# Kernel optimization log

Hardware: AMD Instinct MI355X
Metric: run time of the kernel (lower is better)

## Reference

```python
import jax, jax.numpy as jnp
import numpy as np

WS = 3          # window size (odd)
NH = 8          # num heads
EPS = 1e-5      # LayerNorm eps (torch default)


def _ln(x, g, b):
    mu = x.mean(-1, keepdims=True)
    var = ((x - mu) ** 2).mean(-1, keepdims=True)
    return (x - mu) / jnp.sqrt(var + EPS) * g + b


def _neighbors(x, ws):
    # x: [B,D,H,W,C] -> [B,D,H,W,ws^3,C] zero-padded cubic neighborhoods
    B, D, H, W, C = x.shape
    r = ws // 2
    xp = jnp.pad(x, ((0, 0), (r, r), (r, r), (r, r), (0, 0)))
    slabs = [xp[:, i:i + D, j:j + H, k:k + W, :]
             for i in range(ws) for j in range(ws) for k in range(ws)]
    return jnp.stack(slabs, axis=4)


def _mask(D, H, W, ws):
    # True for valid (in-bounds, non-center) neighbors: [D,H,W,ws^3]
    r = ws // 2
    valid = jnp.pad(jnp.ones((D, H, W), dtype=bool), ((r, r), (r, r), (r, r)))
    slabs = [valid[i:i + D, j:j + H, k:k + W]
             for i in range(ws) for j in range(ws) for k in range(ws)]
    m = jnp.stack(slabs, axis=3)
    center = r * ws * ws + r * ws + r  # self voxel is masked out
    return m.at[..., center].set(False)


def setup_inputs() -> dict:
    key = jax.random.key(0)
    ks = jax.random.split(key, 18)
    B, D, H, W, C = 2, 16, 16, 16, 256
    F = 4 * C
    s = 0.02
    inp = {
        "x": jax.random.normal(ks[0], (B, D, H, W, C), jnp.float32),
        "Wq": jax.random.normal(ks[1], (C, C), jnp.float32) * s,
        "bq": jnp.zeros((C,), jnp.float32),
        "Wk": jax.random.normal(ks[2], (C, C), jnp.float32) * s,
        "bk": jnp.zeros((C,), jnp.float32),
        "Wv": jax.random.normal(ks[3], (C, C), jnp.float32) * s,
        "bv": jnp.zeros((C,), jnp.float32),
        "Wo": jax.random.normal(ks[4], (C, C), jnp.float32) * s,
        "bo": jnp.zeros((C,), jnp.float32),
        "g1": jnp.ones((C,), jnp.float32),
        "b1": jnp.zeros((C,), jnp.float32),
        "g2": jnp.ones((C,), jnp.float32),
        "b2": jnp.zeros((C,), jnp.float32),
        "W1": jax.random.normal(ks[5], (C, F), jnp.float32) * s,
        "bf1": jnp.zeros((F,), jnp.float32),
        "W2": jax.random.normal(ks[6], (F, C), jnp.float32) * s,
        "bf2": jnp.zeros((C,), jnp.float32),
    }
    return inp


def reference(x, Wq, bq, Wk, bk, Wv, bv, Wo, bo, g1, b1, g2, b2, W1, bf1, W2, bf2):
    B, D, H, W, C = x.shape
    ws, nh = WS, NH
    hd = C // nh
    K = ws ** 3

    nb = _neighbors(x, ws)                                   # [B,D,H,W,K,C]
    m = _mask(D, H, W, ws)                                   # [D,H,W,K]

    tn = _ln(x, g1, b1)                                      # norm1 on target only
    q = (tn @ Wq + bq).reshape(B, D, H, W, nh, hd)
    k = (nb @ Wk + bk).reshape(B, D, H, W, K, nh, hd)        # keys from RAW neighbors
    v = (nb @ Wv + bv).reshape(B, D, H, W, K, nh, hd)

    scale = hd ** -0.5
    scores = jnp.einsum('bpqrne,bpqrkne->bpqrnk', q, k) * scale  # [B,D,H,W,nh,K]
    mb = m[None, :, :, :, None, :]
    scores = jnp.where(mb, scores, -jnp.inf)
    attn = jax.nn.softmax(scores, axis=-1)
    attn = jnp.where(jnp.isnan(attn), jnp.zeros_like(attn), attn)

    ao = jnp.einsum('bpqrnk,bpqrkne->bpqrne', attn, v).reshape(B, D, H, W, C)
    ao = ao @ Wo + bo

    t = x + ao                                                # residual (dropout = eval identity)
    h = jax.nn.gelu(_ln(t, g2, b2) @ W1 + bf1, approximate=False) @ W2 + bf2
    return t + h
```

## Files before the change

### kernel.cpp

```cpp
#include <hip/hip_runtime.h>

typedef __bf16 bf16x8 __attribute__((ext_vector_type(8)));
typedef float f32x4 __attribute__((ext_vector_type(4)));

#define DEV static __device__ __forceinline__

DEV unsigned short f2b(float f){
    unsigned int u = __float_as_uint(f);
    u += 0x7fffu + ((u >> 16) & 1u);
    return (unsigned short)(u >> 16);
}
DEV float b2f(unsigned short h){ return __uint_as_float(((unsigned int)h) << 16); }
DEV float blo(unsigned int u){ return __uint_as_float(u << 16); }
DEV float bhi(unsigned int u){ return __uint_as_float(u & 0xffff0000u); }
DEV float gelu_f(float x){ return 0.5f * x * (1.0f + erff(x * 0.7071067811865476f)); }

DEV void gload16(const unsigned short* g, unsigned short* l){
    __builtin_amdgcn_global_load_lds(
        (const __attribute__((address_space(1))) void*)g,
        (__attribute__((address_space(3))) void*)l, 16, 0, 0);
}

static constexpr int NROW = 8192;
static constexpr int C    = 256;
static constexpr int F    = 1024;
static constexpr float ATT_SCALE = 0.17677669529663688f;

__global__ __launch_bounds__(256)
void prep_ln_kernel(const float* __restrict__ Wq, const float* __restrict__ Wk,
                    const float* __restrict__ Wv, const float* __restrict__ Wo,
                    const float* __restrict__ W1, const float* __restrict__ W2,
                    const float* __restrict__ bq, const float* __restrict__ bk,
                    const float* __restrict__ bv,
                    unsigned short* __restrict__ WQT, unsigned short* __restrict__ WKT,
                    unsigned short* __restrict__ WVT, unsigned short* __restrict__ WOT,
                    unsigned short* __restrict__ W1T, unsigned short* __restrict__ W2T,
                    float* __restrict__ bqkv,
                    const float* __restrict__ x, const float* __restrict__ g1,
                    const float* __restrict__ b1,
                    unsigned short* __restrict__ tn, unsigned short* __restrict__ xb)
{
    const int tid = threadIdx.x;
    if (blockIdx.x < 192) {
        __shared__ unsigned short T[64][66];
        const int t = blockIdx.x;
        const float* src; unsigned short* dst;
        int ldw, ldt, r0, c0; float sc = 1.0f;
        if (t < 64) {
            const int m = t >> 4, sub = t & 15;
            src = (m == 0) ? Wq : (m == 1) ? Wk : (m == 2) ? Wv : Wo;
            dst = (m == 0) ? WQT : (m == 1) ? WKT : (m == 2) ? WVT : WOT;
            if (m == 0) sc = ATT_SCALE;
            ldw = 256; ldt = 256;
            r0 = (sub >> 2) * 64; c0 = (sub & 3) * 64;
        } else if (t < 128) {
            const int sub = t - 64;
            src = W1; dst = W1T; ldw = 1024; ldt = 256;
            r0 = (sub >> 4) * 64; c0 = (sub & 15) * 64;
        } else {
            const int sub = t - 128;
            src = W2; dst = W2T; ldw = 256; ldt = 1024;
            r0 = (sub >> 2) * 64; c0 = (sub & 3) * 64;
        }
        #pragma unroll
        for (int i = 0; i < 16; ++i) {
            const int rl = i * 4 + (tid >> 6), cl = tid & 63;
            T[rl][cl] = f2b(src[(size_t)(r0 + rl) * ldw + c0 + cl] * sc);
        }
        __syncthreads();
        #pragma unroll
        for (int j = 0; j < 16; ++j) {
            const int cl = j * 4 + (tid >> 6), rl = tid & 63;
            dst[(size_t)(c0 + cl) * ldt + r0 + rl] = T[rl][cl];
        }
    } else if (blockIdx.x == 192) {
        #pragma unroll
        for (int i = 0; i < 3; ++i) {
            const int v = i * 256 + tid;
            bqkv[v] = (v < 256) ? bq[v] * ATT_SCALE
                    : (v < 512) ? bk[v - 256] : bv[v - 512];
        }
    } else {
        const int row  = (blockIdx.x - 193) * 4 + (tid >> 6);
        const int lane = tid & 63;
        float4 v = ((const float4*)(x + (size_t)row * C))[lane];
        float s = v.x + v.y + v.z + v.w;
        #pragma unroll
        for (int m = 32; m >= 1; m >>= 1) s += __shfl_xor(s, m);
        const float mean = s * (1.0f / 256.0f);
        const float d0 = v.x - mean, d1 = v.y - mean, d2 = v.z - mean, d3 = v.w - mean;
        float s2 = d0 * d0 + d1 * d1 + d2 * d2 + d3 * d3;
        #pragma unroll
        for (int m = 32; m >= 1; m >>= 1) s2 += __shfl_xor(s2, m);
        const float rstd = rsqrtf(s2 * (1.0f / 256.0f) + 1e-5f);
        float4 gg = ((const float4*)g1)[lane];
        float4 bb = ((const float4*)b1)[lane];
        ushort4 o = { f2b(d0 * rstd * gg.x + bb.x), f2b(d1 * rstd * gg.y + bb.y),
                      f2b(d2 * rstd * gg.z + bb.z), f2b(d3 * rstd * gg.w + bb.w) };
        ((ushort4*)(tn + (size_t)row * C))[lane] = o;
        ushort4 xo = { f2b(v.x), f2b(v.y), f2b(v.z), f2b(v.w) };
        ((ushort4*)(xb + (size_t)row * C))[lane] = xo;
    }
}

__global__ __launch_bounds__(256)
void ln_kernel(const float* __restrict__ X, const float* __restrict__ g,
               const float* __restrict__ bta, unsigned short* __restrict__ OUT)
{
    const int row  = blockIdx.x * 4 + (threadIdx.x >> 6);
    const int lane = threadIdx.x & 63;
    float4 v = ((const float4*)(X + (size_t)row * C))[lane];
    float s = v.x + v.y + v.z + v.w;
    #pragma unroll
    for (int m = 32; m >= 1; m >>= 1) s += __shfl_xor(s, m);
    const float mean = s * (1.0f / 256.0f);
    const float d0 = v.x - mean, d1 = v.y - mean, d2 = v.z - mean, d3 = v.w - mean;
    float s2 = d0 * d0 + d1 * d1 + d2 * d2 + d3 * d3;
    #pragma unroll
    for (int m = 32; m >= 1; m >>= 1) s2 += __shfl_xor(s2, m);
    const float rstd = rsqrtf(s2 * (1.0f / 256.0f) + 1e-5f);
    float4 gg = ((const float4*)g)[lane];
    float4 bb = ((const float4*)bta)[lane];
    ushort4 o = { f2b(d0 * rstd * gg.x + bb.x), f2b(d1 * rstd * gg.y + bb.y),
                  f2b(d2 * rstd * gg.z + bb.z), f2b(d3 * rstd * gg.w + bb.w) };
    ((ushort4*)(OUT + (size_t)row * C))[lane] = o;
}

template<int K, int MODE>
DEV void gemm_body(const unsigned short* __restrict__ A, int m0,
                   const unsigned short* __restrict__ BTt,
                   const float* __restrict__ biast,
                   const float* __restrict__ res, void* __restrict__ outp,
                   int ldo, int ocol0,
                   unsigned short (&As)[2][4096], unsigned short (&Bs)[2][4096])
{
    constexpr int BK = 64, NKT = K / BK;
    const int tid  = threadIdx.x;
    const int lane = tid & 63, wid = tid >> 6;
    const int srow = tid >> 3;
    const int schk = (tid & 7) ^ (srow & 7);

    const unsigned short* Ag = A   + (size_t)(m0 + srow) * K + schk * 8;
    const unsigned short* Bg = BTt + (size_t)srow        * K + schk * 8;

    const int wbase = __builtin_amdgcn_readfirstlane(wid) * 512;

    gload16(Ag,          &As[0][wbase]);
    gload16(Ag + 32 * K, &As[0][wbase + 2048]);
    gload16(Bg,          &Bs[0][wbase]);
    gload16(Bg + 32 * K, &Bs[0][wbase + 2048]);
    __syncthreads();

    f32x4 acc[4] = {};
    const int lr = lane & 15, lk = lane >> 4;
    const int sw = lr & 7;

    for (int kt = 0; kt < NKT; ++kt) {
        if (kt + 1 < NKT) {
            const int nb = (kt + 1) & 1;
            gload16(Ag + (kt + 1) * BK,          &As[nb][wbase]);
            gload16(Ag + 32 * K + (kt + 1) * BK, &As[nb][wbase + 2048]);
            gload16(Bg + (kt + 1) * BK,          &Bs[nb][wbase]);
            gload16(Bg + 32 * K + (kt + 1) * BK, &Bs[nb][wbase + 2048]);
        }
        const unsigned short* as = As[kt & 1];
        const unsigned short* bs = Bs[kt & 1];
        #pragma unroll
        for (int s = 0; s < 2; ++s) {
            const int c16 = (s * 4 + lk) ^ sw;
            bf16x8 bfr = *reinterpret_cast<const bf16x8*>(&bs[(wid * 16 + lr) * 64 + c16 * 8]);
            #pragma unroll
            for (int m = 0; m < 4; ++m) {
                bf16x8 afr = *reinterpret_cast<const bf16x8*>(&as[(m * 16 + lr) * 64 + c16 * 8]);
                acc[m] = __builtin_amdgcn_mfma_f32_16x16x32_bf16(afr, bfr, acc[m], 0, 0, 0);
            }
        }
        if (kt + 1 < NKT) __syncthreads();
    }

    const int col  = ocol0 + wid * 16 + lr;
    const float bcol = biast[wid * 16 + lr];
    #pragma unroll
    for (int m = 0; m < 4; ++m) {
        #pragma unroll
        for (int r = 0; r < 4; ++r) {
            const int row = m0 + m * 16 + lk * 4 + r;
            float v = acc[m][r] + bcol;
            if (MODE == 0) {
                ((unsigned short*)outp)[(size_t)row * ldo + col] = f2b(v);
            } else if (MODE == 1) {
                ((unsigned short*)outp)[(size_t)row * ldo + col] = f2b(gelu_f(v));
            } else {
                v += res[(size_t)row * ldo + col];
                ((float*)outp)[(size_t)row * ldo + col] = v;
            }
        }
    }
}

template<int NC, int TS>
DEV void tile_map(int& m0, int& n0){
    const int nwg = gridDim.x;
    const int lin = blockIdx.x;
    const int tile = (lin & 7) * (nwg >> 3) + (lin >> 3);
    m0 = (tile / NC) * TS;
    n0 = (tile % NC) * TS;
}

__global__ __launch_bounds__(256)
void qkv_kernel(const unsigned short* __restrict__ tn,
                const unsigned short* __restrict__ xb,
                const unsigned short* __restrict__ WT,
                const float* __restrict__ bqkv,
                unsigned short* __restrict__ QKV)
{
    __shared__ unsigned short As[2][4096], Bs[2][4096];
    int m0, n0; tile_map<12, 64>(m0, n0);
    const unsigned short* A = (n0 < 256) ? tn : xb;
    gemm_body<256, 0>(A, m0, WT + (size_t)n0 * 256,
                      bqkv + n0, nullptr, QKV, 768, n0, As, Bs);
}

template<int K, int MODE, int NC>
__global__ __launch_bounds__(256)
void gemm_kernel(const unsigned short* __restrict__ A,
                 const unsigned short* __restrict__ BT,
                 const float* __restrict__ bias,
                 const float* __restrict__ res,
                 void* __restrict__ outp, int ldo)
{
    __shared__ unsigned short As[2][4096], Bs[2][4096];
    int m0, n0; tile_map<NC, 64>(m0, n0);
    gemm_body<K, MODE>(A, m0, BT + (size_t)n0 * K,
                       bias + n0, res, outp, ldo, n0, As, Bs);
}

DEV float dot8(uint4 u, const float* q){
    float s;
    s = q[0] * blo(u.x);          s = fmaf(q[1], bhi(u.x), s);
    s = fmaf(q[2], blo(u.y), s);  s = fmaf(q[3], bhi(u.y), s);
    s = fmaf(q[4], blo(u.z), s);  s = fmaf(q[5], bhi(u.z), s);
    s = fmaf(q[6], blo(u.w), s);  s = fmaf(q[7], bhi(u.w), s);
    return s;
}

__global__ __launch_bounds__(256, 4)
void attn_kernel(const unsigned short* __restrict__ QKV,
                 unsigned short* __restrict__ AO)
{
    const int t   = blockIdx.x * 256 + threadIdx.x;
    const int vox = t >> 5;
    const int ch  = (t & 31) * 8;
    const int d = (vox >> 8) & 15, h = (vox >> 4) & 15, w = vox & 15;

    float q[8];
    {
        uint4 u = *reinterpret_cast<const uint4*>(&QKV[(size_t)vox * 768 + ch]);
        q[0]=blo(u.x); q[1]=bhi(u.x); q[2]=blo(u.y); q[3]=bhi(u.y);
        q[4]=blo(u.z); q[5]=bhi(u.z); q[6]=blo(u.w); q[7]=bhi(u.w);
    }

    int nr[27];
    unsigned vm = 0;
    #pragma unroll
    for (int kk = 0; kk < 27; ++kk) {
        const int di = kk / 9 - 1, hi2 = (kk / 3) % 3 - 1, wi = kk % 3 - 1;
        const int nd = d + di, nh = h + hi2, nw = w + wi;
        const bool valid = (kk != 13) && ((unsigned)nd < 16u) &&
                           ((unsigned)nh < 16u) && ((unsigned)nw < 16u);
        nr[kk] = valid ? ((vox & 4096) | (nd << 8) | (nh << 4) | nw) : vox;
        vm |= (unsigned)valid << kk;
    }

    float sc[27];
    #pragma unroll
    for (int g = 0; g < 3; ++g) {
        uint4 ku[9];
        #pragma unroll
        for (int j = 0; j < 9; ++j)
            ku[j] = *reinterpret_cast<const uint4*>(
                &QKV[(size_t)nr[g * 9 + j] * 768 + 256 + ch]);
        #pragma unroll
        for (int j = 0; j < 9; ++j) {
            float s = dot8(ku[j], q);
            s += __shfl_xor(s, 1);
            s += __shfl_xor(s, 2);
            sc[g * 9 + j] = ((vm >> (g * 9 + j)) & 1u) ? s : -INFINITY;
        }
    }

    float mx = sc[0];
    #pragma unroll
    for (int kk = 1; kk < 27; ++kk) mx = fmaxf(mx, sc[kk]);
    float z = 0.0f;
    #pragma unroll
    for (int kk = 0; kk < 27; ++kk) { float p = __expf(sc[kk] - mx); sc[kk] = p; z += p; }
    const float inv = 1.0f / z;

    float acc[8] = {};
    #pragma unroll
    for (int g = 0; g < 3; ++g) {
        uint4 vu[9];
        #pragma unroll
        for (int j = 0; j < 9; ++j)
            vu[j] = *reinterpret_cast<const uint4*>(
                &QKV[(size_t)nr[g * 9 + j] * 768 + 512 + ch]);
        #pragma unroll
        for (int j = 0; j < 9; ++j) {
            const float p = sc[g * 9 + j];
            const uint4 u = vu[j];
            acc[0] = fmaf(p, blo(u.x), acc[0]); acc[1] = fmaf(p, bhi(u.x), acc[1]);
            acc[2] = fmaf(p, blo(u.y), acc[2]); acc[3] = fmaf(p, bhi(u.y), acc[3]);
            acc[4] = fmaf(p, blo(u.z), acc[4]); acc[5] = fmaf(p, bhi(u.z), acc[5]);
            acc[6] = fmaf(p, blo(u.w), acc[6]); acc[7] = fmaf(p, bhi(u.w), acc[7]);
        }
    }

    uint4 o;
    o.x = (unsigned)f2b(acc[0] * inv) | ((unsigned)f2b(acc[1] * inv) << 16);
    o.y = (unsigned)f2b(acc[2] * inv) | ((unsigned)f2b(acc[3] * inv) << 16);
    o.z = (unsigned)f2b(acc[4] * inv) | ((unsigned)f2b(acc[5] * inv) << 16);
    o.w = (unsigned)f2b(acc[6] * inv) | ((unsigned)f2b(acc[7] * inv) << 16);
    *reinterpret_cast<uint4*>(&AO[(size_t)vox * C + ch]) = o;
}

extern "C" void kernel_launch(void* const* d_in, const int* in_sizes, int n_in,
                              void* d_out, int out_size, void* d_ws, size_t ws_size,
                              hipStream_t stream)
{
    const float* x   = (const float*)d_in[0];
    const float* Wq  = (const float*)d_in[1];
    const float* bq  = (const float*)d_in[2];
    const float* Wk  = (const float*)d_in[3];
    const float* bk  = (const float*)d_in[4];
    const float* Wv  = (const float*)d_in[5];
    const float* bv  = (const float*)d_in[6];
    const float* Wo  = (const float*)d_in[7];
    const float* bo  = (const float*)d_in[8];
    const float* g1  = (const float*)d_in[9];
    const float* b1  = (const float*)d_in[10];
    const float* g2  = (const float*)d_in[11];
    const float* b2  = (const float*)d_in[12];
    const float* W1  = (const float*)d_in[13];
    const float* bf1 = (const float*)d_in[14];
    const float* W2  = (const float*)d_in[15];
    const float* bf2 = (const float*)d_in[16];

    char* ws = (char*)d_ws;
    size_t o = 0;
    unsigned short* WQT = (unsigned short*)(ws + o); o += (size_t)256 * 256 * 2;
    unsigned short* WKT = (unsigned short*)(ws + o); o += (size_t)256 * 256 * 2;
    unsigned short* WVT = (unsigned short*)(ws + o); o += (size_t)256 * 256 * 2;
    unsigned short* WOT = (unsigned short*)(ws + o); o += (size_t)256 * 256 * 2;
    unsigned short* W1T = (unsigned short*)(ws + o); o += (size_t)256 * 1024 * 2;
    unsigned short* W2T = (unsigned short*)(ws + o); o += (size_t)1024 * 256 * 2;
    float*          bqkv= (float*)(ws + o);          o += (size_t)768 * 4;
    unsigned short* tn  = (unsigned short*)(ws + o); o += (size_t)NROW * C * 2;
    unsigned short* xb  = (unsigned short*)(ws + o); o += (size_t)NROW * C * 2;
    unsigned short* QKVb= (unsigned short*)(ws + o); o += (size_t)NROW * 768 * 2;
    unsigned short* AOb = (unsigned short*)(ws + o); o += (size_t)NROW * C * 2;
    float*          Tf  = (float*)(ws + o);          o += (size_t)NROW * C * 4;
    unsigned short* tn2 = (unsigned short*)(ws + o); o += (size_t)NROW * C * 2;
    unsigned short* Hb  = (unsigned short*)(ws + o); o += (size_t)NROW * F * 2;

    prep_ln_kernel<<<193 + NROW / 4, 256, 0, stream>>>(Wq, Wk, Wv, Wo, W1, W2, bq, bk, bv,
                                                       WQT, WKT, WVT, WOT, W1T, W2T, bqkv,
                                                       x, g1, b1, tn, xb);

    qkv_kernel<<<(NROW / 64) * 12, 256, 0, stream>>>(tn, xb, WQT, bqkv, QKVb);

    attn_kernel<<<NROW * 32 / 256, 256, 0, stream>>>(QKVb, AOb);

    gemm_kernel<256, 2, 4><<<(NROW / 64) * 4, 256, 0, stream>>>(AOb, WOT, bo, x, Tf, 256);

    ln_kernel<<<NROW / 4, 256, 0, stream>>>(Tf, g2, b2, tn2);

    gemm_kernel<256, 1, 16><<<(NROW / 64) * 16, 256, 0, stream>>>(tn2, W1T, bf1, nullptr, Hb, 1024);

    gemm_kernel<1024, 2, 4><<<(NROW / 64) * 4, 256, 0, stream>>>(Hb, W2T, bf2, Tf, (float*)d_out, 256);
}
```

Before: 79.78 us.

## Widen QKV/W1 GEMM tiles to 64x128 and stream softmax per neighbor slab

```diff
diff --git a/kernel.cpp b/kernel.cpp
--- a/kernel.cpp
+++ b/kernel.cpp
@@ -198,6 +198,91 @@
     }
 }
 
+template<int K, int MODE>
+DEV void gemm_bodyN128(const unsigned short* __restrict__ A, int m0,
+                       const unsigned short* __restrict__ BTt,
+                       const float* __restrict__ biast,
+                       const float* __restrict__ res, void* __restrict__ outp,
+                       int ldo, int ocol0,
+                       unsigned short (&As)[2][4096], unsigned short (&Bs)[2][8192])
+{
+    constexpr int BK = 64, NKT = K / BK;
+    const int tid  = threadIdx.x;
+    const int lane = tid & 63, wid = tid >> 6;
+    const int srow = tid >> 3;
+    const int schk = (tid & 7) ^ (srow & 7);
+
+    const unsigned short* Ag = A   + (size_t)(m0 + srow) * K + schk * 8;
+    const unsigned short* Bg = BTt + (size_t)srow        * K + schk * 8;
+
+    const int wbase = __builtin_amdgcn_readfirstlane(wid) * 512;
+
+    gload16(Ag,          &As[0][wbase]);
+    gload16(Ag + 32 * K, &As[0][wbase + 2048]);
+    #pragma unroll
+    for (int i = 0; i < 4; ++i)
+        gload16(Bg + (size_t)(32 * i) * K, &Bs[0][i * 2048 + wbase]);
+    __syncthreads();
+
+    f32x4 acc[4][2] = {};
+    const int lr = lane & 15, lk = lane >> 4;
+    const int sw = lr & 7;
+    const int brow = wid * 32;
+
+    for (int kt = 0; kt < NKT; ++kt) {
+        if (kt + 1 < NKT) {
+            const int nb = (kt + 1) & 1;
+            gload16(Ag + (kt + 1) * BK,          &As[nb][wbase]);
+            gload16(Ag + 32 * K + (kt + 1) * BK, &As[nb][wbase + 2048]);
+            #pragma unroll
+            for (int i = 0; i < 4; ++i)
+                gload16(Bg + (size_t)(32 * i) * K + (kt + 1) * BK, &Bs[nb][i * 2048 + wbase]);
+        }
+        const unsigned short* as = As[kt & 1];
+        const unsigned short* bs = Bs[kt & 1];
+        #pragma unroll
+        for (int ks = 0; ks < 2; ++ks) {
+            const int c16 = (ks * 4 + lk) ^ sw;
+            bf16x8 af[4], bf[2];
+            #pragma unroll
+            for (int m = 0; m < 4; ++m)
+                af[m] = *reinterpret_cast<const bf16x8*>(&as[(m * 16 + lr) * 64 + c16 * 8]);
+            #pragma unroll
+            for (int n = 0; n < 2; ++n)
+                bf[n] = *reinterpret_cast<const bf16x8*>(&bs[(brow + n * 16 + lr) * 64 + c16 * 8]);
+            #pragma unroll
+            for (int m = 0; m < 4; ++m)
+                #pragma unroll
+                for (int n = 0; n < 2; ++n)
+                    acc[m][n] = __builtin_amdgcn_mfma_f32_16x16x32_bf16(af[m], bf[n], acc[m][n], 0, 0, 0);
+        }
+        if (kt + 1 < NKT) __syncthreads();
+    }
+
+    #pragma unroll
+    for (int n = 0; n < 2; ++n) {
+        const int cl  = brow + n * 16 + lr;
+        const int col = ocol0 + cl;
+        const float bcol = biast[cl];
+        #pragma unroll
+        for (int m = 0; m < 4; ++m) {
+            #pragma unroll
+            for (int r = 0; r < 4; ++r) {
+                const int row = m0 + m * 16 + lk * 4 + r;
+                float v = acc[m][n][r] + bcol;
+                if (MODE == 0) {
+                    ((unsigned short*)outp)[(size_t)row * ldo + col] = f2b(v);
+                } else if (MODE == 1) {
+                    ((unsigned short*)outp)[(size_t)row * ldo + col] = f2b(gelu_f(v));
+                } else {
+                    v += res[(size_t)row * ldo + col];
+                    ((float*)outp)[(size_t)row * ldo + col] = v;
+                }
+            }
+        }
+    }
+}
+
 template<int NC, int TS>
 DEV void tile_map(int& m0, int& n0){
     const int nwg = gridDim.x;
@@ -206,19 +291,39 @@
     m0 = (tile / NC) * TS;
     n0 = (tile % NC) * TS;
 }
-
-__global__ __launch_bounds__(256)
+template<int NC, int TSM, int TSN>
+DEV void tile_map2(int& m0, int& n0){
+    const int nwg = gridDim.x;
+    const int lin = blockIdx.x;
+    const int tile = (lin & 7) * (nwg >> 3) + (lin >> 3);
+    m0 = (tile / NC) * TSM;
+    n0 = (tile % NC) * TSN;
+}
+
+__global__ __launch_bounds__(256, 3)
 void qkv_kernel(const unsigned short* __restrict__ tn,
                 const unsigned short* __restrict__ xb,
                 const unsigned short* __restrict__ WT,
                 const float* __restrict__ bqkv,
                 unsigned short* __restrict__ QKV)
 {
-    __shared__ unsigned short As[2][4096], Bs[2][4096];
-    int m0, n0; tile_map<12, 64>(m0, n0);
+    __shared__ unsigned short As[2][4096], Bs[2][8192];
+    int m0, n0; tile_map2<6, 64, 128>(m0, n0);
     const unsigned short* A = (n0 < 256) ? tn : xb;
-    gemm_body<256, 0>(A, m0, WT + (size_t)n0 * 256,
-                      bqkv + n0, nullptr, QKV, 768, n0, As, Bs);
+    gemm_bodyN128<256, 0>(A, m0, WT + (size_t)n0 * 256,
+                          bqkv + n0, nullptr, QKV, 768, n0, As, Bs);
+}
+
+__global__ __launch_bounds__(256, 3)
+void w1_kernel(const unsigned short* __restrict__ tn2,
+               const unsigned short* __restrict__ W1T,
+               const float* __restrict__ bf1,
+               unsigned short* __restrict__ Hb)
+{
+    __shared__ unsigned short As[2][4096], Bs[2][8192];
+    int m0, n0; tile_map2<8, 64, 128>(m0, n0);
+    gemm_bodyN128<256, 1>(tn2, m0, W1T + (size_t)n0 * 256,
+                          bf1 + n0, nullptr, Hb, 1024, n0, As, Bs);
 }
 
 template<int K, int MODE, int NC>
@@ -260,54 +365,61 @@
         q[4]=blo(u.z); q[5]=bhi(u.z); q[6]=blo(u.w); q[7]=bhi(u.w);
     }
 
-    int nr[27];
-    unsigned vm = 0;
-    #pragma unroll
-    for (int kk = 0; kk < 27; ++kk) {
-        const int di = kk / 9 - 1, hi2 = (kk / 3) % 3 - 1, wi = kk % 3 - 1;
-        const int nd = d + di, nh = h + hi2, nw = w + wi;
-        const bool valid = (kk != 13) && ((unsigned)nd < 16u) &&
-                           ((unsigned)nh < 16u) && ((unsigned)nw < 16u);
-        nr[kk] = valid ? ((vox & 4096) | (nd << 8) | (nh << 4) | nw) : vox;
-        vm |= (unsigned)valid << kk;
-    }
-
-    float sc[27];
+    float mrun = -1e30f, z = 0.0f;
+    float acc[8] = {};
+
     #pragma unroll
     for (int g = 0; g < 3; ++g) {
+        const int di = g - 1;
+        const int nd = d + di;
+        int r9[9];
+        unsigned vm = 0;
+        #pragma unroll
+        for (int j = 0; j < 9; ++j) {
+            const int hi2 = j / 3 - 1, wi = j % 3 - 1;
+            const int nh = h + hi2, nw = w + wi;
+            const bool valid = !(di == 0 && hi2 == 0 && wi == 0) &&
+                               ((unsigned)nd < 16u) && ((unsigned)nh < 16u) &&
+                               ((unsigned)nw < 16u);
+            r9[j] = valid ? ((vox & 4096) | (nd << 8) | (nh << 4) | nw) : vox;
+            vm |= (unsigned)valid << j;
+        }
+
         uint4 ku[9];
         #pragma unroll
         for (int j = 0; j < 9; ++j)
             ku[j] = *reinterpret_cast<const uint4*>(
-                &QKV[(size_t)nr[g * 9 + j] * 768 + 256 + ch]);
+                &QKV[(size_t)r9[j] * 768 + 256 + ch]);
+
+        float s9[9];
         #pragma unroll
         for (int j = 0; j < 9; ++j) {
             float s = dot8(ku[j], q);
             s += __shfl_xor(s, 1);
             s += __shfl_xor(s, 2);
-            sc[g * 9 + j] = ((vm >> (g * 9 + j)) & 1u) ? s : -INFINITY;
-        }
-    }
-
-    float mx = sc[0];
-    #pragma unroll
-    for (int kk = 1; kk < 27; ++kk) mx = fmaxf(mx, sc[kk]);
-    float z = 0.0f;
-    #pragma unroll
-    for (int kk = 0; kk < 27; ++kk) { float p = __expf(sc[kk] - mx); sc[kk] = p; z += p; }
-    const float inv = 1.0f / z;
-
-    float acc[8] = {};
-    #pragma unroll
-    for (int g = 0; g < 3; ++g) {
+            s9[j] = ((vm >> j) & 1u) ? s : -INFINITY;
+        }
+
+        float gm = s9[0];
+        #pragma unroll
+        for (int j = 1; j < 9; ++j) gm = fmaxf(gm, s9[j]);
+        const float nm = fmaxf(mrun, gm);
+        const float rs = __expf(mrun - nm);
+        mrun = nm;
+        z *= rs;
+        #pragma unroll
+        for (int i = 0; i < 8; ++i) acc[i] *= rs;
+
         uint4 vu[9];
         #pragma unroll
         for (int j = 0; j < 9; ++j)
             vu[j] = *reinterpret_cast<const uint4*>(
-                &QKV[(size_t)nr[g * 9 + j] * 768 + 512 + ch]);
+                &QKV[(size_t)r9[j] * 768 + 512 + ch]);
+
         #pragma unroll
         for (int j = 0; j < 9; ++j) {
-            const float p = sc[g * 9 + j];
+            const float p = __expf(s9[j] - nm);
+            z += p;
             const uint4 u = vu[j];
             acc[0] = fmaf(p, blo(u.x), acc[0]); acc[1] = fmaf(p, bhi(u.x), acc[1]);
             acc[2] = fmaf(p, blo(u.y), acc[2]); acc[3] = fmaf(p, bhi(u.y), acc[3]);
@@ -316,6 +428,7 @@
         }
     }
 
+    const float inv = 1.0f / z;
     uint4 o;
     o.x = (unsigned)f2b(acc[0] * inv) | ((unsigned)f2b(acc[1] * inv) << 16);
     o.y = (unsigned)f2b(acc[2] * inv) | ((unsigned)f2b(acc[3] * inv) << 16);
@@ -367,7 +480,7 @@
                                                        WQT, WKT, WVT, WOT, W1T, W2T, bqkv,
                                                        x, g1, b1, tn, xb);
 
-    qkv_kernel<<<(NROW / 64) * 12, 256, 0, stream>>>(tn, xb, WQT, bqkv, QKVb);
+    qkv_kernel<<<(NROW / 64) * 6, 256, 0, stream>>>(tn, xb, WQT, bqkv, QKVb);
 
     attn_kernel<<<NROW * 32 / 256, 256, 0, stream>>>(QKVb, AOb);
 
@@ -375,7 +488,7 @@
 
     ln_kernel<<<NROW / 4, 256, 0, stream>>>(Tf, g2, b2, tn2);
 
-    gemm_kernel<256, 1, 16><<<(NROW / 64) * 16, 256, 0, stream>>>(tn2, W1T, bf1, nullptr, Hb, 1024);
+    w1_kernel<<<(NROW / 64) * 8, 256, 0, stream>>>(tn2, W1T, bf1, Hb);
 
     gemm_kernel<1024, 2, 4><<<(NROW / 64) * 4, 256, 0, stream>>>(Hb, W2T, bf2, Tf, (float*)d_out, 256);
 }
```

Measured after the change: 74.97 us. -6.0%, faster.
